# Kernel optimization log

Measured on AMD Instinct MI355X. Metric: run time of the kernel, lower is better.

The kernel has to match this reference:

```python
import jax, jax.numpy as jnp
import numpy as np

B, S, D = 2, 1024, 2048
H, KVH, HD = 16, 4, 128
HID, E, K = 4096, 8, 2
EPS = 1e-5
NEG = -1e9  # finite stand-in for -inf in the causal mask


def setup_inputs() -> dict:
    key = jax.random.key(0)
    ks = jax.random.split(key, 16)
    sc = 0.02
    x = jax.random.normal(ks[0], (B, S, D), jnp.float32)
    # rotary tables (theta = 10000), as cos/sin instead of complex
    inv_freq = 1.0 / (10000.0 ** (jnp.arange(0, HD, 2, dtype=jnp.float32) / HD))
    t = jnp.arange(S, dtype=jnp.float32)
    fr = jnp.outer(t, inv_freq)  # [S, HD/2]
    freqs_cos, freqs_sin = jnp.cos(fr), jnp.sin(fr)
    positions = jnp.arange(S, dtype=jnp.int32)
    mask = jnp.where(jnp.tril(jnp.ones((S, S), bool)), 0.0, NEG).astype(jnp.float32)
    attn_norm_w = jnp.ones((D,), jnp.float32)
    ffn_norm_w = jnp.ones((D,), jnp.float32)
    wq = jax.random.normal(ks[1], (D, H * HD), jnp.float32) * sc
    wk = jax.random.normal(ks[2], (D, KVH * HD), jnp.float32) * sc
    wv = jax.random.normal(ks[3], (D, KVH * HD), jnp.float32) * sc
    wo = jax.random.normal(ks[4], (H * HD, D), jnp.float32) * sc
    gate_w = jax.random.normal(ks[5], (D, E), jnp.float32) * sc
    w1 = jax.random.normal(ks[6], (E, D, HID), jnp.float32) * sc
    w2 = jax.random.normal(ks[7], (E, HID, D), jnp.float32) * sc
    w3 = jax.random.normal(ks[8], (E, D, HID), jnp.float32) * sc
    return dict(x=x, freqs_cos=freqs_cos, freqs_sin=freqs_sin, positions=positions,
                mask=mask, attn_norm_w=attn_norm_w, ffn_norm_w=ffn_norm_w,
                wq=wq, wk=wk, wv=wv, wo=wo, gate_w=gate_w, w1=w1, w2=w2, w3=w3)


def rmsnorm(x, w):
    xf = x.astype(jnp.float32)
    n = xf * jax.lax.rsqrt(jnp.mean(xf * xf, axis=-1, keepdims=True) + EPS)
    return n.astype(x.dtype) * w


def rope(t, cos, sin):
    # t: [B,S,nh,HD]; interleaved (real, imag) pairs like torch.view_as_complex
    tr = t.reshape(*t.shape[:-1], HD // 2, 2)
    xr, xi = tr[..., 0], tr[..., 1]
    c = cos[None, :, None, :]
    s = sin[None, :, None, :]
    out = jnp.stack([xr * c - xi * s, xr * s + xi * c], axis=-1)
    return out.reshape(t.shape)


def block_fwd(x, freqs_cos, freqs_sin, mask, attn_norm_w, ffn_norm_w,
              wq, wk, wv, wo, gate_w, w1, w2, w3):
    # ---- attention ----
    h = rmsnorm(x, attn_norm_w)
    q = (h @ wq).reshape(B, S, H, HD)
    k = (h @ wk).reshape(B, S, KVH, HD)
    v = (h @ wv).reshape(B, S, KVH, HD)
    q = rope(q, freqs_cos, freqs_sin)
    k = rope(k, freqs_cos, freqs_sin)
    rep = H // KVH
    k = jnp.repeat(k, rep, axis=2)  # [B,S,H,HD]
    v = jnp.repeat(v, rep, axis=2)
    scale = HD ** -0.5
    scores = jnp.einsum('bqhd,bkhd->bhqk', q, k) * scale + mask[None, None]
    probs = jax.nn.softmax(scores.astype(jnp.float32), axis=-1).astype(q.dtype)
    attn = jnp.einsum('bhqk,bkhd->bqhd', probs, v).reshape(B, S, H * HD)
    h1 = x + attn @ wo
    # ---- MoE FFN ----
    t = rmsnorm(h1, ffn_norm_w).reshape(-1, D)  # [T,D]
    logits = t @ gate_w  # [T,E]
    topw, sel = jax.lax.top_k(logits, K)
    topw = jax.nn.softmax(topw.astype(jnp.float32), axis=-1).astype(t.dtype)
    out = jnp.zeros_like(t)
    for i in range(E):
        coef = jnp.sum(jnp.where(sel == i, topw, 0.0), axis=-1, keepdims=True)  # [T,1]
        ff = (jax.nn.silu(t @ w1[i]) * (t @ w3[i])) @ w2[i]
        out = out + coef * ff
    return h1 + out.reshape(B, S, D)


def reference(x, freqs_cos, freqs_sin, positions, mask, attn_norm_w, ffn_norm_w,
              wq, wk, wv, wo, gate_w, w1, w2, w3):
    # prefill branch (positions.shape[0] > 1): KV-cache scatter is a write-only
    # side effect in the original and does not affect this output.
    del positions
    return block_fwd(x, freqs_cos, freqs_sin, mask, attn_norm_w, ffn_norm_w,
                     wq, wk, wv, wo, gate_w, w1, w2, w3)
```

## Files before the change

kernel.cpp:

```cpp
#include <hip/hip_runtime.h>

typedef unsigned short u16;
typedef unsigned int u32;
typedef __bf16 bf16x8 __attribute__((ext_vector_type(8)));
typedef _Float16 f16;
typedef f16 f16x8 __attribute__((ext_vector_type(8)));
typedef float f32x4 __attribute__((ext_vector_type(4)));
typedef u32 u32x2 __attribute__((ext_vector_type(2)));

#define DEVFN __device__ __forceinline__

constexpr int kB = 2, kS = 1024, kD = 2048, kH = 16, kKVH = 4, kHD = 128;
constexpr int kHID = 4096, kE = 8;
constexpr int kRows = kB * kS;
constexpr int kQKVN = kH*kHD + 2*kKVH*kHD;
constexpr int kSlotsPad = 5120;
constexpr int kMaxTiles = 40;
constexpr float kEps = 1e-5f;
constexpr float kNeg = -1000000000.0f;
constexpr float kScale = 0.08838834764831845f;

DEVFN u16 f2bf(float f) {
  u32 u = __float_as_uint(f);
  return (u16)((u + 0x7fffu + ((u >> 16) & 1u)) >> 16);
}
DEVFN float bf2f(u16 u) { u32 v = ((u32)u) << 16; return __uint_as_float(v); }

DEVFN void split8v(float4 a, float4 b, f16x8& hi, f16x8& lo) {
  float v[8] = {a.x, a.y, a.z, a.w, b.x, b.y, b.z, b.w};
  #pragma unroll
  for (int e = 0; e < 8; ++e) {
    f16 h = (f16)v[e];
    hi[e] = h;
    lo[e] = (f16)(v[e] - (float)h);
  }
}

DEVFN void gll16(const void* g, void* l) {
  __builtin_amdgcn_global_load_lds(
      (const __attribute__((address_space(1))) void*)g,
      (__attribute__((address_space(3))) void*)l, 16, 0, 0);
}

DEVFN u32x2 pk4bf(float a, float b, float c, float d) {
  union { __bf16 h[4]; u32x2 w; } u;
  u.h[0] = (__bf16)a; u.h[1] = (__bf16)b;
  u.h[2] = (__bf16)c; u.h[3] = (__bf16)d;
  return u.w;
}

__global__ __launch_bounds__(256) void rms_split_kernel(const float* __restrict__ in,
    const float* __restrict__ w, f16* __restrict__ oh, f16* __restrict__ ol) {
  int row = blockIdx.x, tid = threadIdx.x;
  const float* x = in + (size_t)row * kD;
  float4 v0 = *(const float4*)&x[tid*8];
  float4 v1 = *(const float4*)&x[tid*8+4];
  float ss = v0.x*v0.x+v0.y*v0.y+v0.z*v0.z+v0.w*v0.w
           + v1.x*v1.x+v1.y*v1.y+v1.z*v1.z+v1.w*v1.w;
  #pragma unroll
  for (int off = 32; off; off >>= 1) ss += __shfl_xor(ss, off);
  __shared__ float red[4];
  if ((tid & 63) == 0) red[tid >> 6] = ss;
  __syncthreads();
  float tot = red[0] + red[1] + red[2] + red[3];
  float rs = rsqrtf(tot * (1.0f/kD) + kEps);
  float4 w0 = *(const float4*)&w[tid*8];
  float4 w1 = *(const float4*)&w[tid*8+4];
  float4 o0, o1;
  o0.x = v0.x*rs*w0.x; o0.y = v0.y*rs*w0.y; o0.z = v0.z*rs*w0.z; o0.w = v0.w*rs*w0.w;
  o1.x = v1.x*rs*w1.x; o1.y = v1.y*rs*w1.y; o1.z = v1.z*rs*w1.z; o1.w = v1.w*rs*w1.w;
  f16x8 hi, lo;
  split8v(o0, o1, hi, lo);
  *(f16x8*)&oh[(size_t)row*kD + tid*8] = hi;
  *(f16x8*)&ol[(size_t)row*kD + tid*8] = lo;
}

__global__ __launch_bounds__(256) void rms_bf16_kernel(const float* __restrict__ in,
    const float* __restrict__ w, u16* __restrict__ out) {
  int row = blockIdx.x, tid = threadIdx.x;
  const float* x = in + (size_t)row * kD;
  float4 v0 = *(const float4*)&x[tid*8];
  float4 v1 = *(const float4*)&x[tid*8+4];
  float ss = v0.x*v0.x+v0.y*v0.y+v0.z*v0.z+v0.w*v0.w
           + v1.x*v1.x+v1.y*v1.y+v1.z*v1.z+v1.w*v1.w;
  #pragma unroll
  for (int off = 32; off; off >>= 1) ss += __shfl_xor(ss, off);
  __shared__ float red[4];
  if ((tid & 63) == 0) red[tid >> 6] = ss;
  __syncthreads();
  float tot = red[0] + red[1] + red[2] + red[3];
  float rs = rsqrtf(tot * (1.0f/kD) + kEps);
  float4 w0 = *(const float4*)&w[tid*8];
  float4 w1 = *(const float4*)&w[tid*8+4];
  union { int4 i4; u16 u[8]; } pk;
  pk.u[0] = f2bf(v0.x*rs*w0.x); pk.u[1] = f2bf(v0.y*rs*w0.y);
  pk.u[2] = f2bf(v0.z*rs*w0.z); pk.u[3] = f2bf(v0.w*rs*w0.w);
  pk.u[4] = f2bf(v1.x*rs*w1.x); pk.u[5] = f2bf(v1.y*rs*w1.y);
  pk.u[6] = f2bf(v1.z*rs*w1.z); pk.u[7] = f2bf(v1.w*rs*w1.w);
  *(int4*)&out[(size_t)row*kD + tid*8] = pk.i4;
}

__global__ void transpose_split_kernel(const float* __restrict__ in,
    f16* __restrict__ hi, f16* __restrict__ lo, int R, int C, int noff, int ldout) {
  __shared__ float tile[32][33];
  int c0 = blockIdx.x * 32, r0 = blockIdx.y * 32;
  int tx = threadIdx.x, ty = threadIdx.y;
  #pragma unroll
  for (int i = 0; i < 32; i += 8)
    tile[ty + i][tx] = in[(size_t)(r0 + ty + i) * C + c0 + tx];
  __syncthreads();
  #pragma unroll
  for (int i = 0; i < 32; i += 8) {
    float v = tile[tx][ty + i];
    f16 h = (f16)v;
    size_t o = (size_t)(noff + c0 + ty + i) * ldout + r0 + tx;
    hi[o] = h;
    lo[o] = (f16)(v - (float)h);
  }
}

__global__ void vt_split_kernel(const float* __restrict__ qkv,
    f16* __restrict__ vTh, f16* __restrict__ vTl) {
  __shared__ float tile[32][33];
  int s0 = blockIdx.x * 32, c0 = blockIdx.y * 32, b = blockIdx.z;
  int tx = threadIdx.x, ty = threadIdx.y;
  #pragma unroll
  for (int i = 0; i < 32; i += 8)
    tile[ty + i][tx] = qkv[(size_t)(b*kS + s0 + ty + i) * kQKVN + kH*kHD + kKVH*kHD + c0 + tx];
  __syncthreads();
  #pragma unroll
  for (int i = 0; i < 32; i += 8) {
    float v = tile[tx][ty + i];
    f16 h = (f16)v;
    size_t o = (size_t)(b*kKVH*kHD + c0 + ty + i) * kS + s0 + tx;
    vTh[o] = h;
    vTl[o] = (f16)(v - (float)h);
  }
}

template<bool ADDX>
__global__ __launch_bounds__(256) void gemm_sf16_kernel(
    const f16* __restrict__ Ah0, const f16* __restrict__ Al0, int lda,
    const f16* __restrict__ Bh0, const f16* __restrict__ Bl0,
    float* __restrict__ C, int ldc, int coff,
    const float* __restrict__ X, int ldx, int K) {
  __shared__ __align__(16) u16 Ah[128*64], Al[128*64], Bh[128*64], Bl[128*64];
  int tid = threadIdx.x, lane = tid & 63, w = tid >> 6;
  int bm = blockIdx.y * 128, bn = blockIdx.x * 128;
  int wr = w >> 1, wc = w & 1;
  int hg = lane >> 4, lid = lane & 15;
  f32x4 acc[4][4] = {};
  const f16 *aH[4], *aL[4], *bH[4], *bL[4];
  #pragma unroll
  for (int j = 0; j < 4; ++j) {
    int r = w*32 + j*8 + (lane >> 3);
    int colc = ((lane & 7) ^ (r & 7)) * 8;
    aH[j] = Ah0 + (size_t)(bm + r) * lda + colc;
    aL[j] = Al0 + (size_t)(bm + r) * lda + colc;
    bH[j] = Bh0 + (size_t)(bn + r) * K + colc;
    bL[j] = Bl0 + (size_t)(bn + r) * K + colc;
  }
  const char* AhB = (const char*)Ah; const char* AlB = (const char*)Al;
  const char* BhB = (const char*)Bh; const char* BlB = (const char*)Bl;
  for (int kt = 0; kt < K; kt += 64) {
    __syncthreads();
    #pragma unroll
    for (int j = 0; j < 4; ++j) {
      int lb = w*2048 + j*512;
      gll16(aH[j] + kt, &Ah[lb]);
      gll16(aL[j] + kt, &Al[lb]);
      gll16(bH[j] + kt, &Bh[lb]);
      gll16(bL[j] + kt, &Bl[lb]);
    }
    __syncthreads();
    #pragma unroll
    for (int kk = 0; kk < 2; ++kk) {
      f16x8 ah[4], al[4], bh[4], bl[4];
      #pragma unroll
      for (int f = 0; f < 4; ++f) {
        int rA = wr*64 + f*16 + lid;
        int oA = (rA*128 + kk*64 + hg*16) ^ ((rA & 7) << 4);
        ah[f] = *(const f16x8*)(AhB + oA);
        al[f] = *(const f16x8*)(AlB + oA);
        int rB = wc*64 + f*16 + lid;
        int oB = (rB*128 + kk*64 + hg*16) ^ ((rB & 7) << 4);
        bh[f] = *(const f16x8*)(BhB + oB);
        bl[f] = *(const f16x8*)(BlB + oB);
      }
      __builtin_amdgcn_s_setprio(1);
      #pragma unroll
      for (int i = 0; i < 4; ++i)
        #pragma unroll
        for (int j = 0; j < 4; ++j) {
          acc[i][j] = __builtin_amdgcn_mfma_f32_16x16x32_f16(ah[i], bh[j], acc[i][j], 0, 0, 0);
          acc[i][j] = __builtin_amdgcn_mfma_f32_16x16x32_f16(ah[i], bl[j], acc[i][j], 0, 0, 0);
          acc[i][j] = __builtin_amdgcn_mfma_f32_16x16x32_f16(al[i], bh[j], acc[i][j], 0, 0, 0);
        }
      __builtin_amdgcn_s_setprio(0);
    }
  }
  #pragma unroll
  for (int i = 0; i < 4; ++i) {
    #pragma unroll
    for (int rr = 0; rr < 4; ++rr) {
      size_t gr = (size_t)(bm + wr*64 + i*16 + hg*4 + rr);
      #pragma unroll
      for (int j = 0; j < 4; ++j) {
        int gc = bn + wc*64 + j*16 + lid;
        float v = acc[i][j][rr];
        if (ADDX) v += X[gr * ldx + gc];
        C[gr * ldc + coff + gc] = v;
      }
    }
  }
}

__global__ __launch_bounds__(256) void rope_kernel(float* __restrict__ qkv,
    const float* __restrict__ fc, const float* __restrict__ fs,
    f16* __restrict__ Kh, f16* __restrict__ Kl) {
  int idx = blockIdx.x * 256 + threadIdx.x;
  constexpr int NQ = kB*kS*kH*(kHD/2);
  constexpr int NK = kB*kS*kKVH*(kHD/2);
  if (idx < NQ) {
    int i = idx & 63, h = (idx >> 6) & 15, s = (idx >> 10) & 1023, b = idx >> 20;
    size_t base = ((size_t)(b*kS + s))*kQKVN + h*kHD + 2*i;
    float c = fc[s*64 + i], sn = fs[s*64 + i];
    float xr = qkv[base], xi = qkv[base+1];
    qkv[base]   = xr*c - xi*sn;
    qkv[base+1] = xr*sn + xi*c;
  } else {
    int j = idx - NQ; if (j >= NK) return;
    int i = j & 63, h = (j >> 6) & 3, s = (j >> 8) & 1023, b = j >> 18;
    size_t src = ((size_t)(b*kS + s))*kQKVN + kH*kHD + h*kHD + 2*i;
    float c = fc[s*64 + i], sn = fs[s*64 + i];
    float xr = qkv[src], xi = qkv[src+1];
    float o0 = xr*c - xi*sn, o1 = xr*sn + xi*c;
    size_t dst = (((size_t)(b*kKVH + h))*kS + s)*kHD + 2*i;
    f16 h0 = (f16)o0, h1 = (f16)o1;
    Kh[dst]   = h0; Kl[dst]   = (f16)(o0 - (float)h0);
    Kh[dst+1] = h1; Kl[dst+1] = (f16)(o1 - (float)h1);
  }
}

__global__ __launch_bounds__(256) void attn_sf16_kernel(const float* __restrict__ qkv,
    const f16* __restrict__ Ksh, const f16* __restrict__ Ksl,
    const f16* __restrict__ vTh, const f16* __restrict__ vTl,
    f16* __restrict__ outh, f16* __restrict__ outl) {
  int qt = (int)gridDim.x - 1 - blockIdx.x;
  int h = blockIdx.y, b = blockIdx.z;
  int kvh = h >> 2;
  int q0 = qt * 64;
  __shared__ __align__(16) char Kh[64*128*2], Kl[64*128*2];
  __shared__ __align__(16) char Vh[128*64*2], Vl[128*64*2];
  __shared__ __align__(16) char Ph[4][16*64*2], Pl[4][16*64*2];
  int tid = threadIdx.x, lane = tid & 63, w = tid >> 6;
  int hg = lane >> 4, lid = lane & 15;

  f16x8 qh[4], ql[4];
  {
    const float* qrow = qkv + (size_t)(b*kS + q0 + w*16 + lid) * kQKVN + h*kHD;
    #pragma unroll
    for (int ks = 0; ks < 4; ++ks) {
      float4 a = *(const float4*)(qrow + ks*32 + hg*8);
      float4 c = *(const float4*)(qrow + ks*32 + hg*8 + 4);
      split8v(a, c, qh[ks], ql[ks]);
    }
  }
  f32x4 oacc[8] = {};
  float m[4] = {-3.0e38f, -3.0e38f, -3.0e38f, -3.0e38f};
  float lsum[4] = {};
  char* Phw = Ph[w];
  char* Plw = Pl[w];

  for (int kt = 0; kt <= qt; ++kt) {
    __syncthreads();
    {
      int r = tid >> 2, c0 = (tid & 3) * 32;
      const f16* khr = Ksh + ((size_t)(b*kKVH + kvh)*kS + kt*64 + r) * kHD + c0;
      const f16* klr = Ksl + ((size_t)(b*kKVH + kvh)*kS + kt*64 + r) * kHD + c0;
      #pragma unroll
      for (int s8 = 0; s8 < 4; ++s8) {
        int4 hi = *(const int4*)(khr + s8*8);
        int4 lo = *(const int4*)(klr + s8*8);
        int off = (r*256 + c0*2 + s8*16) ^ ((r & 7) << 4);
        *(int4*)(Kh + off) = hi;
        *(int4*)(Kl + off) = lo;
      }
    }
    {
      int r = tid >> 1, c0 = (tid & 1) * 32;
      const f16* vhr = vTh + (size_t)(b*kKVH*kHD + kvh*kHD + r) * kS + kt*64 + c0;
      const f16* vlr = vTl + (size_t)(b*kKVH*kHD + kvh*kHD + r) * kS + kt*64 + c0;
      #pragma unroll
      for (int s8 = 0; s8 < 4; ++s8) {
        int4 hi = *(const int4*)(vhr + s8*8);
        int4 lo = *(const int4*)(vlr + s8*8);
        int off = (r*128 + c0*2 + s8*16) ^ ((r & 7) << 4);
        *(int4*)(Vh + off) = hi;
        *(int4*)(Vl + off) = lo;
      }
    }
    __syncthreads();

    f32x4 sacc[4] = {};
    __builtin_amdgcn_s_setprio(1);
    #pragma unroll
    for (int ks = 0; ks < 4; ++ks) {
      #pragma unroll
      for (int j = 0; j < 4; ++j) {
        int rB = j*16 + lid;
        int off = (rB*256 + ks*64 + hg*16) ^ ((rB & 7) << 4);
        f16x8 kh = *(const f16x8*)(Kh + off);
        f16x8 klo = *(const f16x8*)(Kl + off);
        sacc[j] = __builtin_amdgcn_mfma_f32_16x16x32_f16(qh[ks], kh, sacc[j], 0, 0, 0);
        sacc[j] = __builtin_amdgcn_mfma_f32_16x16x32_f16(qh[ks], klo, sacc[j], 0, 0, 0);
        sacc[j] = __builtin_amdgcn_mfma_f32_16x16x32_f16(ql[ks], kh, sacc[j], 0, 0, 0);
      }
    }
    __builtin_amdgcn_s_setprio(0);
    float s[4][4], ps[4][4];
    bool diag = (kt == qt);
    #pragma unroll
    for (int j = 0; j < 4; ++j)
      #pragma unroll
      for (int r = 0; r < 4; ++r) {
        float v = sacc[j][r] * kScale;
        if (diag) {
          int kvabs = kt*64 + j*16 + lid;
          int qabs = q0 + w*16 + hg*4 + r;
          if (kvabs > qabs) v = kNeg;
        }
        s[j][r] = v;
      }
    float pm[4], cf[4];
    #pragma unroll
    for (int r = 0; r < 4; ++r) {
      pm[r] = fmaxf(fmaxf(s[0][r], s[1][r]), fmaxf(s[2][r], s[3][r]));
      #pragma unroll
      for (int msk = 1; msk < 16; msk <<= 1) pm[r] = fmaxf(pm[r], __shfl_xor(pm[r], msk));
      float mn = fmaxf(m[r], pm[r]);
      cf[r] = __expf(m[r] - mn);
      m[r] = mn;
    }
    #pragma unroll
    for (int j2 = 0; j2 < 8; ++j2)
      #pragma unroll
      for (int r = 0; r < 4; ++r) oacc[j2][r] *= cf[r];
    float rs[4] = {};
    #pragma unroll
    for (int j = 0; j < 4; ++j)
      #pragma unroll
      for (int r = 0; r < 4; ++r) {
        float p = __expf(s[j][r] - m[r]);
        ps[j][r] = p;
        rs[r] += p;
      }
    #pragma unroll
    for (int r = 0; r < 4; ++r) lsum[r] = lsum[r]*cf[r] + rs[r];
    #pragma unroll
    for (int j = 0; j < 4; ++j)
      #pragma unroll
      for (int r = 0; r < 4; ++r) {
        int q = hg*4 + r;
        int off = (q*128 + (j*16 + lid)*2) ^ ((q & 7) << 4);
        f16 ph = (f16)ps[j][r];
        *(f16*)(Phw + off) = ph;
        *(f16*)(Plw + off) = (f16)(ps[j][r] - (float)ph);
      }
    #pragma unroll
    for (int kk2 = 0; kk2 < 2; ++kk2) {
      int oP = (lid*128 + kk2*64 + hg*16) ^ ((lid & 7) << 4);
      f16x8 pa_h = *(const f16x8*)(Phw + oP);
      f16x8 pa_l = *(const f16x8*)(Plw + oP);
      __builtin_amdgcn_s_setprio(1);
      #pragma unroll
      for (int j2 = 0; j2 < 8; ++j2) {
        int rV = j2*16 + lid;
        int off = (rV*128 + kk2*64 + hg*16) ^ ((rV & 7) << 4);
        f16x8 vh = *(const f16x8*)(Vh + off);
        f16x8 vl = *(const f16x8*)(Vl + off);
        oacc[j2] = __builtin_amdgcn_mfma_f32_16x16x32_f16(pa_h, vh, oacc[j2], 0, 0, 0);
        oacc[j2] = __builtin_amdgcn_mfma_f32_16x16x32_f16(pa_h, vl, oacc[j2], 0, 0, 0);
        oacc[j2] = __builtin_amdgcn_mfma_f32_16x16x32_f16(pa_l, vh, oacc[j2], 0, 0, 0);
      }
      __builtin_amdgcn_s_setprio(0);
    }
  }
  #pragma unroll
  for (int r = 0; r < 4; ++r) {
    #pragma unroll
    for (int msk = 1; msk < 16; msk <<= 1) lsum[r] += __shfl_xor(lsum[r], msk);
    lsum[r] = 1.f / lsum[r];
  }
  #pragma unroll
  for (int j2 = 0; j2 < 8; ++j2)
    #pragma unroll
    for (int r = 0; r < 4; ++r) {
      size_t o = (size_t)(b*kS + q0 + w*16 + hg*4 + r) * kD + h*kHD + j2*16 + lid;
      float v = oacc[j2][r] * lsum[r];
      f16 hh = (f16)v;
      outh[o] = hh;
      outl[o] = (f16)(v - (float)hh);
    }
}

__global__ void zero_counts_kernel(int* counts) {
  if (threadIdx.x < kE) counts[threadIdx.x] = 0;
}

__global__ __launch_bounds__(64) void gate_kernel(const float* __restrict__ h1,
    const float* __restrict__ wn, const float* __restrict__ gw,
    int* __restrict__ packA, int* __restrict__ packB,
    float* __restrict__ cA, float* __restrict__ cB,
    int* __restrict__ lists, int* __restrict__ counts) {
  int row = blockIdx.x, lane = threadIdx.x;
  const float* x = h1 + (size_t)row * kD;
  float ss = 0.f;
  for (int d = lane; d < kD; d += 64) { float v = x[d]; ss = fmaf(v, v, ss); }
  #pragma unroll
  for (int off = 32; off; off >>= 1) ss += __shfl_xor(ss, off);
  float rs = rsqrtf(ss * (1.0f/kD) + kEps);
  float acc[kE] = {};
  for (int d = lane; d < kD; d += 64) {
    float g = x[d] * rs * wn[d];
    const float* gr = gw + (size_t)d * kE;
    #pragma unroll
    for (int e = 0; e < kE; ++e) acc[e] = fmaf(g, gr[e], acc[e]);
  }
  #pragma unroll
  for (int e = 0; e < kE; ++e)
    #pragma unroll
    for (int off = 32; off; off >>= 1) acc[e] += __shfl_xor(acc[e], off);
  if (lane == 0) {
    int i1 = 0; float l1 = acc[0];
    #pragma unroll
    for (int e = 1; e < kE; ++e) if (acc[e] > l1) { l1 = acc[e]; i1 = e; }
    int i2 = -1; float l2 = -3.4e38f;
    #pragma unroll
    for (int e = 0; e < kE; ++e) if (e != i1 && acc[e] > l2) { l2 = acc[e]; i2 = e; }
    float e2 = __expf(l2 - l1);
    float inv = 1.f / (1.f + e2);
    int p1 = atomicAdd(&counts[i1], 1); lists[i1*kRows + p1] = row;
    int p2 = atomicAdd(&counts[i2], 1); lists[i2*kRows + p2] = row;
    packA[row] = i1*2048 + p1; cA[row] = inv;
    packB[row] = i2*2048 + p2; cB[row] = e2 * inv;
  }
}

__global__ void prefix_kernel(const int* __restrict__ counts,
    int* __restrict__ padbase, int* __restrict__ tileTab) {
  if (threadIdx.x == 0) {
    int base = 0, idx = 0;
    for (int e = 0; e < kE; ++e) {
      padbase[e] = base;
      int nt = (counts[e] + 127) >> 7;
      for (int t = 0; t < nt; ++t) tileTab[idx++] = (e << 8) | t;
      base += nt << 7;
    }
    for (; idx < kMaxTiles; ++idx) tileTab[idx] = -1;
  }
}

__global__ __launch_bounds__(256) void gemm_up_kernel(
    const u16* __restrict__ A, const float* __restrict__ W1, const float* __restrict__ W3,
    u16* __restrict__ hid, const int* __restrict__ lists,
    const int* __restrict__ counts, const int* __restrict__ padbase,
    const int* __restrict__ tileTab) {
  int tab = tileTab[blockIdx.y];
  if (tab < 0) return;
  int e = tab >> 8, mb = tab & 255;
  int cnt = counts[e];
  int bm = mb * 128;
  int slot0 = padbase[e] + bm;
  const int* ids = lists + e * kRows;
  int g = blockIdx.x;
  __shared__ __align__(16) char SM[65536];
  u16* As[2]   = { (u16*)SM, (u16*)(SM + 16384) };
  char* B1s[2] = { SM + 32768, SM + 40960 };
  char* B3s[2] = { SM + 49152, SM + 57344 };
  int tid = threadIdx.x, lane = tid & 63, w = tid >> 6;
  int wr = w >> 1, wc = w & 1;
  int hg = lane >> 4, lid = lane & 15;
  f32x4 acc[4][4] = {};

  const u16* aP[4];
  #pragma unroll
  for (int j = 0; j < 4; ++j) {
    int r = w*32 + j*8 + (lane >> 3);
    int colc = ((lane & 7) ^ (r & 7)) * 8;
    int rr = bm + r; if (rr >= cnt) rr = cnt - 1;
    aP[j] = A + (size_t)ids[rr] * kD + colc;
  }
  const float* b1e = W1 + (size_t)e*kD*kHID + (size_t)g*64 + lane;
  const float* b3e = W3 + (size_t)e*kD*kHID + (size_t)g*64 + lane;
  int wOff[4];
  #pragma unroll
  for (int s = 0; s < 4; ++s)
    wOff[s] = (lane*128 + s*32 + w*8) ^ ((lane & 7) << 4);

  auto stageA = [&](int buf, int t) {
    int kt = t * 64;
    #pragma unroll
    for (int j = 0; j < 4; ++j) gll16(aP[j] + kt, &As[buf][w*2048 + j*512]);
  };
  float r1v[4][4], r3v[4][4];
  auto loadB = [&](int t) {
    int kt = t * 64;
    #pragma unroll
    for (int s = 0; s < 4; ++s)
      #pragma unroll
      for (int j = 0; j < 4; ++j) {
        size_t ko = (size_t)(kt + s*16 + w*4 + j) * kHID;
        r1v[s][j] = b1e[ko];
        r3v[s][j] = b3e[ko];
      }
  };
  auto writeB = [&](int buf) {
    #pragma unroll
    for (int s = 0; s < 4; ++s) {
      *(u32x2*)(B1s[buf] + wOff[s]) = pk4bf(r1v[s][0], r1v[s][1], r1v[s][2], r1v[s][3]);
      *(u32x2*)(B3s[buf] + wOff[s]) = pk4bf(r3v[s][0], r3v[s][1], r3v[s][2], r3v[s][3]);
    }
  };
  auto compute = [&](int buf) {
    const char* AsB = (const char*)As[buf];
    const char* Bb = wc ? B3s[buf] : B1s[buf];
    #pragma unroll
    for (int kk = 0; kk < 2; ++kk) {
      bf16x8 af[4], bfv[4];
      #pragma unroll
      for (int f = 0; f < 4; ++f) {
        int rA = wr*64 + f*16 + lid;
        af[f] = *(const bf16x8*)(AsB + ((rA*128 + kk*64 + hg*16) ^ ((rA & 7) << 4)));
        int rB = f*16 + lid;
        bfv[f] = *(const bf16x8*)(Bb + ((rB*128 + kk*64 + hg*16) ^ ((rB & 7) << 4)));
      }
      __builtin_amdgcn_s_setprio(1);
      #pragma unroll
      for (int i = 0; i < 4; ++i)
        #pragma unroll
        for (int j = 0; j < 4; ++j)
          acc[i][j] = __builtin_amdgcn_mfma_f32_16x16x32_bf16(af[i], bfv[j], acc[i][j], 0, 0, 0);
      __builtin_amdgcn_s_setprio(0);
    }
  };

  constexpr int NT = kD / 64;
  stageA(0, 0);
  loadB(0);
  writeB(0);
  __syncthreads();
  for (int t = 0; t < NT; t += 2) {
    stageA(1, t+1); loadB(t+1);
    compute(0);
    writeB(1);
    __syncthreads();
    if (t+2 < NT) { stageA(0, t+2); loadB(t+2); }
    compute(1);
    if (t+2 < NT) writeB(0);
    __syncthreads();
  }

  float* Xch = (float*)SM;
  if (wc == 0) {
    #pragma unroll
    for (int i = 0; i < 4; ++i)
      #pragma unroll
      for (int rr = 0; rr < 4; ++rr) {
        int row = wr*64 + i*16 + hg*4 + rr;
        #pragma unroll
        for (int j = 0; j < 4; ++j)
          Xch[row*64 + j*16 + lid] = acc[i][j][rr];
      }
  }
  __syncthreads();
  if (wc == 1) {
    #pragma unroll
    for (int i = 0; i < 4; ++i)
      #pragma unroll
      for (int rr = 0; rr < 4; ++rr) {
        int row = wr*64 + i*16 + hg*4 + rr;
        int gr = bm + row;
        if (gr >= cnt) continue;
        u16* orow = hid + (size_t)(slot0 + row) * kHID + g*64;
        #pragma unroll
        for (int j = 0; j < 4; ++j) {
          int col = j*16 + lid;
          float g1 = Xch[row*64 + col];
          float g3 = acc[i][j][rr];
          orow[col] = f2bf(g1 / (1.f + __expf(-g1)) * g3);
        }
      }
  }
}

__global__ __launch_bounds__(256) void gemm_down_kernel(
    const u16* __restrict__ hid, const float* __restrict__ W2,
    u16* __restrict__ ff, const int* __restrict__ padbase,
    const int* __restrict__ tileTab) {
  int tab = tileTab[blockIdx.y];
  if (tab < 0) return;
  int e = tab >> 8, mb = tab & 255;
  int slot0 = padbase[e] + mb * 128;
  int bn = blockIdx.x * 128;
  __shared__ __align__(16) char SM[65536];
  u16* As[2] = { (u16*)SM, (u16*)(SM + 16384) };
  char* Bs[2] = { SM + 32768, SM + 49152 };
  int tid = threadIdx.x, lane = tid & 63, w = tid >> 6;
  int wr = w >> 1, wc = w & 1;
  int hg = lane >> 4, lid = lane & 15;
  f32x4 acc[4][4] = {};

  const u16* aP[4];
  #pragma unroll
  for (int j = 0; j < 4; ++j) {
    int r = w*32 + j*8 + (lane >> 3);
    int colc = ((lane & 7) ^ (r & 7)) * 8;
    aP[j] = hid + (size_t)(slot0 + r) * kHID + colc;
  }
  int nrow = (w & 1)*64 + lane;
  int kq = w >> 1;
  const float* b2e = W2 + (size_t)e*kHID*kD + (size_t)bn + nrow;
  int wOff[8];
  #pragma unroll
  for (int s = 0; s < 8; ++s)
    wOff[s] = (nrow*128 + s*16 + kq*8) ^ ((nrow & 7) << 4);

  auto stageA = [&](int buf, int t) {
    int kt = t * 64;
    #pragma unroll
    for (int j = 0; j < 4; ++j) gll16(aP[j] + kt, &As[buf][w*2048 + j*512]);
  };
  float rbv[8][4];
  auto loadB = [&](int t) {
    int kt = t * 64;
    #pragma unroll
    for (int s = 0; s < 8; ++s)
      #pragma unroll
      for (int j = 0; j < 4; ++j)
        rbv[s][j] = b2e[(size_t)(kt + s*8 + kq*4 + j) * kD];
  };
  auto writeB = [&](int buf) {
    #pragma unroll
    for (int s = 0; s < 8; ++s)
      *(u32x2*)(Bs[buf] + wOff[s]) = pk4bf(rbv[s][0], rbv[s][1], rbv[s][2], rbv[s][3]);
  };
  auto compute = [&](int buf) {
    const char* AsB = (const char*)As[buf];
    const char* Bb = Bs[buf];
    #pragma unroll
    for (int kk = 0; kk < 2; ++kk) {
      bf16x8 af[4], bfv[4];
      #pragma unroll
      for (int f = 0; f < 4; ++f) {
        int rA = wr*64 + f*16 + lid;
        af[f] = *(const bf16x8*)(AsB + ((rA*128 + kk*64 + hg*16) ^ ((rA & 7) << 4)));
        int rB = wc*64 + f*16 + lid;
        bfv[f] = *(const bf16x8*)(Bb + ((rB*128 + kk*64 + hg*16) ^ ((rB & 7) << 4)));
      }
      __builtin_amdgcn_s_setprio(1);
      #pragma unroll
      for (int i = 0; i < 4; ++i)
        #pragma unroll
        for (int j = 0; j < 4; ++j)
          acc[i][j] = __builtin_amdgcn_mfma_f32_16x16x32_bf16(af[i], bfv[j], acc[i][j], 0, 0, 0);
      __builtin_amdgcn_s_setprio(0);
    }
  };

  constexpr int NT = kHID / 64;
  stageA(0, 0);
  loadB(0);
  writeB(0);
  __syncthreads();
  for (int t = 0; t < NT; t += 2) {
    stageA(1, t+1); loadB(t+1);
    compute(0);
    writeB(1);
    __syncthreads();
    if (t+2 < NT) { stageA(0, t+2); loadB(t+2); }
    compute(1);
    if (t+2 < NT) writeB(0);
    __syncthreads();
  }

  #pragma unroll
  for (int i = 0; i < 4; ++i)
    #pragma unroll
    for (int rr = 0; rr < 4; ++rr) {
      int row = wr*64 + i*16 + hg*4 + rr;
      u16* orow = ff + (size_t)(slot0 + row) * kD + bn;
      #pragma unroll
      for (int j = 0; j < 4; ++j)
        orow[wc*64 + j*16 + lid] = f2bf(acc[i][j][rr]);
    }
}

__global__ __launch_bounds__(256) void moe_combine_kernel(
    const u16* __restrict__ ff, const int* __restrict__ padbase,
    const int* __restrict__ packA, const int* __restrict__ packB,
    const float* __restrict__ cA, const float* __restrict__ cB,
    float* __restrict__ outp) {
  int row = blockIdx.x, tid = threadIdx.x;
  int pa = packA[row], pb = packB[row];
  int sa = padbase[pa >> 11] + (pa & 2047);
  int sb = padbase[pb >> 11] + (pb & 2047);
  float ca = cA[row], cb = cB[row];
  union { int4 i4; u16 u[8]; } va, vb;
  va.i4 = *(const int4*)(ff + (size_t)sa * kD + tid*8);
  vb.i4 = *(const int4*)(ff + (size_t)sb * kD + tid*8);
  float* o = outp + (size_t)row * kD + tid*8;
  float4 o0 = *(const float4*)o;
  float4 o1 = *(const float4*)(o + 4);
  o0.x += ca*bf2f(va.u[0]) + cb*bf2f(vb.u[0]);
  o0.y += ca*bf2f(va.u[1]) + cb*bf2f(vb.u[1]);
  o0.z += ca*bf2f(va.u[2]) + cb*bf2f(vb.u[2]);
  o0.w += ca*bf2f(va.u[3]) + cb*bf2f(vb.u[3]);
  o1.x += ca*bf2f(va.u[4]) + cb*bf2f(vb.u[4]);
  o1.y += ca*bf2f(va.u[5]) + cb*bf2f(vb.u[5]);
  o1.z += ca*bf2f(va.u[6]) + cb*bf2f(vb.u[6]);
  o1.w += ca*bf2f(va.u[7]) + cb*bf2f(vb.u[7]);
  *(float4*)o = o0;
  *(float4*)(o + 4) = o1;
}

extern "C" void kernel_launch(void* const* d_in, const int* in_sizes, int n_in,
                              void* d_out, int out_size, void* d_ws, size_t ws_size,
                              hipStream_t stream) {
  const float* x    = (const float*)d_in[0];
  const float* fcos = (const float*)d_in[1];
  const float* fsin = (const float*)d_in[2];
  const float* anw  = (const float*)d_in[5];
  const float* fnw  = (const float*)d_in[6];
  const float* wq   = (const float*)d_in[7];
  const float* wk   = (const float*)d_in[8];
  const float* wv   = (const float*)d_in[9];
  const float* wo   = (const float*)d_in[10];
  const float* gw   = (const float*)d_in[11];
  const float* w1   = (const float*)d_in[12];
  const float* w2   = (const float*)d_in[13];
  const float* w3   = (const float*)d_in[14];
  float* outp = (float*)d_out;

  char* ws = (char*)d_ws;
  size_t off = 0;
  auto alloc = [&](size_t bytes) -> void* {
    void* p = ws + off; off += (bytes + 255) & ~(size_t)255; return p;
  };
  f16* h16h   = (f16*)alloc((size_t)kRows*kD*2);
  f16* h16l   = (f16*)alloc((size_t)kRows*kD*2);
  float* qkv  = (float*)alloc((size_t)kRows*kQKVN*4);
  f16* Ksh    = (f16*)alloc((size_t)kB*kKVH*kS*kHD*2);
  f16* Ksl    = (f16*)alloc((size_t)kB*kKVH*kS*kHD*2);
  f16* vTh    = (f16*)alloc((size_t)kB*kKVH*kHD*kS*2);
  f16* vTl    = (f16*)alloc((size_t)kB*kKVH*kHD*kS*2);
  f16* a16h   = (f16*)alloc((size_t)kRows*kD*2);
  f16* a16l   = (f16*)alloc((size_t)kRows*kD*2);
  u16* tbf    = (u16*)alloc((size_t)kRows*kD*2);
  int* packA  = (int*)alloc(kRows*4);
  int* packB  = (int*)alloc(kRows*4);
  float* cAv  = (float*)alloc(kRows*4);
  float* cBv  = (float*)alloc(kRows*4);
  int* counts = (int*)alloc(kE*4);
  int* padbase= (int*)alloc(kE*4);
  int* tileTab= (int*)alloc(kMaxTiles*4);
  int* lists  = (int*)alloc((size_t)kE*kRows*4);
  f16* Bqh    = (f16*)alloc((size_t)kQKVN*kD*2);
  f16* Bql    = (f16*)alloc((size_t)kQKVN*kD*2);
  f16* Bwh    = (f16*)alloc((size_t)kD*kD*2);
  f16* Bwl    = (f16*)alloc((size_t)kD*kD*2);
  u16* hid    = (u16*)alloc((size_t)kSlotsPad*kHID*2);
  u16* ffb    = (u16*)alloc((size_t)kSlotsPad*kD*2);

  transpose_split_kernel<<<dim3(kD/32, kD/32), dim3(32,8), 0, stream>>>(wq, Bqh, Bql, kD, 2048, 0, kD);
  transpose_split_kernel<<<dim3(512/32, kD/32), dim3(32,8), 0, stream>>>(wk, Bqh, Bql, kD, 512, 2048, kD);
  transpose_split_kernel<<<dim3(512/32, kD/32), dim3(32,8), 0, stream>>>(wv, Bqh, Bql, kD, 512, 2560, kD);
  transpose_split_kernel<<<dim3(kD/32, kD/32), dim3(32,8), 0, stream>>>(wo, Bwh, Bwl, kD, kD, 0, kD);

  rms_split_kernel<<<kRows, 256, 0, stream>>>(x, anw, h16h, h16l);
  gemm_sf16_kernel<false><<<dim3(kQKVN/128, kRows/128), 256, 0, stream>>>(
      h16h, h16l, kD, Bqh, Bql, qkv, kQKVN, 0, nullptr, 0, kD);
  rope_kernel<<<(kB*kS*(kH+kKVH)*(kHD/2))/256, 256, 0, stream>>>(qkv, fcos, fsin, Ksh, Ksl);
  vt_split_kernel<<<dim3(kS/32, (kKVH*kHD)/32, kB), dim3(32,8), 0, stream>>>(qkv, vTh, vTl);
  attn_sf16_kernel<<<dim3(kS/64, kH, kB), 256, 0, stream>>>(qkv, Ksh, Ksl, vTh, vTl, a16h, a16l);
  gemm_sf16_kernel<true><<<dim3(kD/128, kRows/128), 256, 0, stream>>>(
      a16h, a16l, kD, Bwh, Bwl, outp, kD, 0, x, kD, kD);

  zero_counts_kernel<<<1, 64, 0, stream>>>(counts);
  gate_kernel<<<kRows, 64, 0, stream>>>(outp, fnw, gw, packA, packB, cAv, cBv, lists, counts);
  prefix_kernel<<<1, 64, 0, stream>>>(counts, padbase, tileTab);
  rms_bf16_kernel<<<kRows, 256, 0, stream>>>(outp, fnw, tbf);

  gemm_up_kernel<<<dim3(kHID/64, kMaxTiles), 256, 0, stream>>>(
      tbf, w1, w3, hid, lists, counts, padbase, tileTab);
  gemm_down_kernel<<<dim3(kD/128, kMaxTiles), 256, 0, stream>>>(
      hid, w2, ffb, padbase, tileTab);
  moe_combine_kernel<<<kRows, 256, 0, stream>>>(
      ffb, padbase, packA, packB, cAv, cBv, outp);
}
```

Measured before the change: 866.6 us.

## Deepen MoE GEMM weight prefetch with float2 loads and explicit waitcnt barriers

In both MoE expert GEMM kernels, the fp32 weight loads now fetch two adjacent columns per thread as float2, which halves the number of global load instructions. The weights for the next tile are held in two register sets (even and odd), so they are loaded one full tile ahead. The loop uses hand-placed s_barrier calls with explicit vmcnt and lgkmcnt waits and sched_barrier fences, so outstanding global loads can overlap compute instead of draining at every __syncthreads. In exchange this needs more registers, and correctness now depends on the hard-coded vmcnt(20) count matching the real number of loads in flight.

New measurement: 1.134 ms. 30.9% more time.

```diff
diff --git a/kernel.cpp b/kernel.cpp
--- a/kernel.cpp
+++ b/kernel.cpp
@@ -48,6 +48,22 @@
   u.h[2] = (__bf16)c; u.h[3] = (__bf16)d;
   return u.w;
 }
+
+DEVFN void baronly() { __builtin_amdgcn_sched_barrier(0);
+  __builtin_amdgcn_s_barrier();
+  __builtin_amdgcn_sched_barrier(0); }
+DEVFN void barlgkm() { __builtin_amdgcn_sched_barrier(0);
+  asm volatile("s_waitcnt lgkmcnt(0)" ::: "memory");
+  __builtin_amdgcn_s_barrier();
+  __builtin_amdgcn_sched_barrier(0); }
+DEVFN void barvm20() { __builtin_amdgcn_sched_barrier(0);
+  asm volatile("s_waitcnt vmcnt(20) lgkmcnt(0)" ::: "memory");
+  __builtin_amdgcn_s_barrier();
+  __builtin_amdgcn_sched_barrier(0); }
+DEVFN void barvm0() { __builtin_amdgcn_sched_barrier(0);
+  asm volatile("s_waitcnt vmcnt(0) lgkmcnt(0)" ::: "memory");
+  __builtin_amdgcn_s_barrier();
+  __builtin_amdgcn_sched_barrier(0); }
 
 __global__ __launch_bounds__(256) void rms_split_kernel(const float* __restrict__ in,
     const float* __restrict__ w, f16* __restrict__ oh, f16* __restrict__ ol) {
@@ -491,35 +507,39 @@
     int rr = bm + r; if (rr >= cnt) rr = cnt - 1;
     aP[j] = A + (size_t)ids[rr] * kD + colc;
   }
-  const float* b1e = W1 + (size_t)e*kD*kHID + (size_t)g*64 + lane;
-  const float* b3e = W3 + (size_t)e*kD*kHID + (size_t)g*64 + lane;
-  int wOff[4];
-  #pragma unroll
-  for (int s = 0; s < 4; ++s)
-    wOff[s] = (lane*128 + s*32 + w*8) ^ ((lane & 7) << 4);
+  int c0 = (tid & 31) * 2, hk = tid >> 5;
+  const float* b1e = W1 + (size_t)e*kD*kHID + (size_t)g*64 + c0;
+  const float* b3e = W3 + (size_t)e*kD*kHID + (size_t)g*64 + c0;
+  int wOffX[2], wOffY[2];
+  #pragma unroll
+  for (int q = 0; q < 2; ++q) {
+    int k0b = (hk*8 + q*4) * 2;
+    wOffX[q] = (c0*128 + k0b) ^ ((c0 & 7) << 4);
+    wOffY[q] = ((c0+1)*128 + k0b) ^ (((c0+1) & 7) << 4);
+  }
+  float2 r1E[8], r3E[8], r1O[8], r3O[8];
 
   auto stageA = [&](int buf, int t) {
     int kt = t * 64;
     #pragma unroll
     for (int j = 0; j < 4; ++j) gll16(aP[j] + kt, &As[buf][w*2048 + j*512]);
   };
-  float r1v[4][4], r3v[4][4];
-  auto loadB = [&](int t) {
+  auto loadB = [&](float2* r1, float2* r3, int t) {
     int kt = t * 64;
     #pragma unroll
-    for (int s = 0; s < 4; ++s)
-      #pragma unroll
-      for (int j = 0; j < 4; ++j) {
-        size_t ko = (size_t)(kt + s*16 + w*4 + j) * kHID;
-        r1v[s][j] = b1e[ko];
-        r3v[s][j] = b3e[ko];
-      }
+    for (int j = 0; j < 8; ++j) {
+      size_t ko = (size_t)(kt + hk*8 + j) * kHID;
+      r1[j] = *(const float2*)(b1e + ko);
+      r3[j] = *(const float2*)(b3e + ko);
+    }
   };
-  auto writeB = [&](int buf) {
-    #pragma unroll
-    for (int s = 0; s < 4; ++s) {
-      *(u32x2*)(B1s[buf] + wOff[s]) = pk4bf(r1v[s][0], r1v[s][1], r1v[s][2], r1v[s][3]);
-      *(u32x2*)(B3s[buf] + wOff[s]) = pk4bf(r3v[s][0], r3v[s][1], r3v[s][2], r3v[s][3]);
+  auto writeB = [&](int buf, float2* r1, float2* r3) {
+    #pragma unroll
+    for (int q = 0; q < 2; ++q) {
+      *(u32x2*)(B1s[buf] + wOffX[q]) = pk4bf(r1[q*4].x, r1[q*4+1].x, r1[q*4+2].x, r1[q*4+3].x);
+      *(u32x2*)(B1s[buf] + wOffY[q]) = pk4bf(r1[q*4].y, r1[q*4+1].y, r1[q*4+2].y, r1[q*4+3].y);
+      *(u32x2*)(B3s[buf] + wOffX[q]) = pk4bf(r3[q*4].x, r3[q*4+1].x, r3[q*4+2].x, r3[q*4+3].x);
+      *(u32x2*)(B3s[buf] + wOffY[q]) = pk4bf(r3[q*4].y, r3[q*4+1].y, r3[q*4+2].y, r3[q*4+3].y);
     }
   };
   auto compute = [&](int buf) {
@@ -546,20 +566,31 @@
   };
 
   constexpr int NT = kD / 64;
-  stageA(0, 0);
-  loadB(0);
-  writeB(0);
+  stageA(0, 0); stageA(1, 1);
+  loadB(r1E, r3E, 0);
+  loadB(r1O, r3O, 1);
+  writeB(0, r1E, r3E);
+  barlgkm();
+  for (int t = 0; t + 2 < NT; t += 2) {
+    loadB(r1E, r3E, t+2);
+    compute(0);
+    baronly();
+    stageA(0, t+2);
+    writeB(1, r1O, r3O);
+    barvm20();
+    loadB(r1O, r3O, t+3);
+    compute(1);
+    baronly();
+    stageA(1, t+3);
+    writeB(0, r1E, r3E);
+    barvm20();
+  }
+  compute(0);
+  baronly();
+  writeB(1, r1O, r3O);
+  barvm0();
+  compute(1);
   __syncthreads();
-  for (int t = 0; t < NT; t += 2) {
-    stageA(1, t+1); loadB(t+1);
-    compute(0);
-    writeB(1);
-    __syncthreads();
-    if (t+2 < NT) { stageA(0, t+2); loadB(t+2); }
-    compute(1);
-    if (t+2 < NT) writeB(0);
-    __syncthreads();
-  }
 
   float* Xch = (float*)SM;
   if (wc == 0) {
@@ -618,32 +649,34 @@
     int colc = ((lane & 7) ^ (r & 7)) * 8;
     aP[j] = hid + (size_t)(slot0 + r) * kHID + colc;
   }
-  int nrow = (w & 1)*64 + lane;
-  int kq = w >> 1;
-  const float* b2e = W2 + (size_t)e*kHID*kD + (size_t)bn + nrow;
-  int wOff[8];
-  #pragma unroll
-  for (int s = 0; s < 8; ++s)
-    wOff[s] = (nrow*128 + s*16 + kq*8) ^ ((nrow & 7) << 4);
+  int c0 = (tid & 63) * 2, kgrp = tid >> 6;
+  const float* b2e = W2 + (size_t)e*kHID*kD + (size_t)bn + c0;
+  int wOffX[4], wOffY[4];
+  #pragma unroll
+  for (int q = 0; q < 4; ++q) {
+    int k0b = (kgrp*16 + q*4) * 2;
+    wOffX[q] = (c0*128 + k0b) ^ ((c0 & 7) << 4);
+    wOffY[q] = ((c0+1)*128 + k0b) ^ (((c0+1) & 7) << 4);
+  }
+  float2 rE[16], rO[16];
 
   auto stageA = [&](int buf, int t) {
     int kt = t * 64;
     #pragma unroll
     for (int j = 0; j < 4; ++j) gll16(aP[j] + kt, &As[buf][w*2048 + j*512]);
   };
-  float rbv[8][4];
-  auto loadB = [&](int t) {
+  auto loadB = [&](float2* r, int t) {
     int kt = t * 64;
     #pragma unroll
-    for (int s = 0; s < 8; ++s)
-      #pragma unroll
-      for (int j = 0; j < 4; ++j)
-        rbv[s][j] = b2e[(size_t)(kt + s*8 + kq*4 + j) * kD];
+    for (int j = 0; j < 16; ++j)
+      r[j] = *(const float2*)(b2e + (size_t)(kt + kgrp*16 + j) * kD);
   };
-  auto writeB = [&](int buf) {
-    #pragma unroll
-    for (int s = 0; s < 8; ++s)
-      *(u32x2*)(Bs[buf] + wOff[s]) = pk4bf(rbv[s][0], rbv[s][1], rbv[s][2], rbv[s][3]);
+  auto writeB = [&](int buf, float2* r) {
+    #pragma unroll
+    for (int q = 0; q < 4; ++q) {
+      *(u32x2*)(Bs[buf] + wOffX[q]) = pk4bf(r[q*4].x, r[q*4+1].x, r[q*4+2].x, r[q*4+3].x);
+      *(u32x2*)(Bs[buf] + wOffY[q]) = pk4bf(r[q*4].y, r[q*4+1].y, r[q*4+2].y, r[q*4+3].y);
+    }
   };
   auto compute = [&](int buf) {
     const char* AsB = (const char*)As[buf];
@@ -669,20 +702,31 @@
   };
 
   constexpr int NT = kHID / 64;
-  stageA(0, 0);
-  loadB(0);
-  writeB(0);
+  stageA(0, 0); stageA(1, 1);
+  loadB(rE, 0);
+  loadB(rO, 1);
+  writeB(0, rE);
+  barlgkm();
+  for (int t = 0; t + 2 < NT; t += 2) {
+    loadB(rE, t+2);
+    compute(0);
+    baronly();
+    stageA(0, t+2);
+    writeB(1, rO);
+    barvm20();
+    loadB(rO, t+3);
+    compute(1);
+    baronly();
+    stageA(1, t+3);
+    writeB(0, rE);
+    barvm20();
+  }
+  compute(0);
+  baronly();
+  writeB(1, rO);
+  barvm0();
+  compute(1);
   __syncthreads();
-  for (int t = 0; t < NT; t += 2) {
-    stageA(1, t+1); loadB(t+1);
-    compute(0);
-    writeB(1);
-    __syncthreads();
-    if (t+2 < NT) { stageA(0, t+2); loadB(t+2); }
-    compute(1);
-    if (t+2 < NT) writeB(0);
-    __syncthreads();
-  }
 
   #pragma unroll
   for (int i = 0; i < 4; ++i)
```

## Use 8 waves per block in MoE up/down GEMMs with smaller per-wave tiles

Applied to the files above, without the earlier changes.

Doubles the threads per block in the expert up- and down-projection GEMMs from 256 to 512 and re-splits the 128-wide tile so each wave computes a 64x32 sub-tile instead of 64x64. The A-staging and fp32-to-bf16 weight loads are divided over twice as many threads. The aim is more waves in flight to hide the global-load latency of the fp32 weights and fewer registers per thread. In exchange, each wave does less MFMA work per LDS fragment load, and the launch bound of 4 blocks per CU with 64KB of LDS per block may not be reachable.

After: 864.0 us (median of 2 runs). About the same (-0.3%).

```diff
diff --git a/kernel.cpp b/kernel.cpp
--- a/kernel.cpp
+++ b/kernel.cpp
@@ -461,7 +461,7 @@
   }
 }
 
-__global__ __launch_bounds__(256) void gemm_up_kernel(
+__global__ __launch_bounds__(512, 4) void gemm_up_kernel(
     const u16* __restrict__ A, const float* __restrict__ W1, const float* __restrict__ W3,
     u16* __restrict__ hid, const int* __restrict__ lists,
     const int* __restrict__ counts, const int* __restrict__ padbase,
@@ -479,67 +479,70 @@
   char* B1s[2] = { SM + 32768, SM + 40960 };
   char* B3s[2] = { SM + 49152, SM + 57344 };
   int tid = threadIdx.x, lane = tid & 63, w = tid >> 6;
-  int wr = w >> 1, wc = w & 1;
+  int wr = w >> 2, wcc = w & 3;
   int hg = lane >> 4, lid = lane & 15;
-  f32x4 acc[4][4] = {};
-
-  const u16* aP[4];
-  #pragma unroll
-  for (int j = 0; j < 4; ++j) {
-    int r = w*32 + j*8 + (lane >> 3);
+  f32x4 acc[4][2] = {};
+
+  const u16* aP[2];
+  #pragma unroll
+  for (int j = 0; j < 2; ++j) {
+    int r = w*16 + j*8 + (lane >> 3);
     int colc = ((lane & 7) ^ (r & 7)) * 8;
     int rr = bm + r; if (rr >= cnt) rr = cnt - 1;
     aP[j] = A + (size_t)ids[rr] * kD + colc;
   }
   const float* b1e = W1 + (size_t)e*kD*kHID + (size_t)g*64 + lane;
   const float* b3e = W3 + (size_t)e*kD*kHID + (size_t)g*64 + lane;
-  int wOff[4];
-  #pragma unroll
-  for (int s = 0; s < 4; ++s)
-    wOff[s] = (lane*128 + s*32 + w*8) ^ ((lane & 7) << 4);
+  int wOff[2];
+  #pragma unroll
+  for (int s = 0; s < 2; ++s)
+    wOff[s] = (lane*128 + w*16 + s*8) ^ ((lane & 7) << 4);
 
   auto stageA = [&](int buf, int t) {
     int kt = t * 64;
     #pragma unroll
-    for (int j = 0; j < 4; ++j) gll16(aP[j] + kt, &As[buf][w*2048 + j*512]);
+    for (int j = 0; j < 2; ++j) gll16(aP[j] + kt, &As[buf][w*1024 + j*512]);
   };
-  float r1v[4][4], r3v[4][4];
+  float r1v[2][4], r3v[2][4];
   auto loadB = [&](int t) {
     int kt = t * 64;
     #pragma unroll
-    for (int s = 0; s < 4; ++s)
+    for (int s = 0; s < 2; ++s)
       #pragma unroll
       for (int j = 0; j < 4; ++j) {
-        size_t ko = (size_t)(kt + s*16 + w*4 + j) * kHID;
+        size_t ko = (size_t)(kt + w*8 + s*4 + j) * kHID;
         r1v[s][j] = b1e[ko];
         r3v[s][j] = b3e[ko];
       }
   };
   auto writeB = [&](int buf) {
     #pragma unroll
-    for (int s = 0; s < 4; ++s) {
+    for (int s = 0; s < 2; ++s) {
       *(u32x2*)(B1s[buf] + wOff[s]) = pk4bf(r1v[s][0], r1v[s][1], r1v[s][2], r1v[s][3]);
       *(u32x2*)(B3s[buf] + wOff[s]) = pk4bf(r3v[s][0], r3v[s][1], r3v[s][2], r3v[s][3]);
     }
   };
   auto compute = [&](int buf) {
     const char* AsB = (const char*)As[buf];
-    const char* Bb = wc ? B3s[buf] : B1s[buf];
+    const char* Bb = (wcc >= 2) ? B3s[buf] : B1s[buf];
     #pragma unroll
     for (int kk = 0; kk < 2; ++kk) {
-      bf16x8 af[4], bfv[4];
+      bf16x8 af[4], bfv[2];
       #pragma unroll
       for (int f = 0; f < 4; ++f) {
         int rA = wr*64 + f*16 + lid;
         af[f] = *(const bf16x8*)(AsB + ((rA*128 + kk*64 + hg*16) ^ ((rA & 7) << 4)));
-        int rB = f*16 + lid;
+      }
+      #pragma unroll
+      for (int f = 0; f < 2; ++f) {
+        int rB = (wcc & 1)*32 + f*16 + lid;
         bfv[f] = *(const bf16x8*)(Bb + ((rB*128 + kk*64 + hg*16) ^ ((rB & 7) << 4)));
       }
       __builtin_amdgcn_s_setprio(1);
       #pragma unroll
       for (int i = 0; i < 4; ++i)
         #pragma unroll
-        for (int j = 0; j < 4; ++j)
+        for (int j = 0; j < 2; ++j)
           acc[i][j] = __builtin_amdgcn_mfma_f32_16x16x32_bf16(af[i], bfv[j], acc[i][j], 0, 0, 0);
       __builtin_amdgcn_s_setprio(0);
     }
@@ -562,19 +565,19 @@
   }
 
   float* Xch = (float*)SM;
-  if (wc == 0) {
+  if (wcc < 2) {
     #pragma unroll
     for (int i = 0; i < 4; ++i)
       #pragma unroll
       for (int rr = 0; rr < 4; ++rr) {
         int row = wr*64 + i*16 + hg*4 + rr;
         #pragma unroll
-        for (int j = 0; j < 4; ++j)
-          Xch[row*64 + j*16 + lid] = acc[i][j][rr];
+        for (int j = 0; j < 2; ++j)
+          Xch[row*64 + (wcc & 1)*32 + j*16 + lid] = acc[i][j][rr];
       }
   }
   __syncthreads();
-  if (wc == 1) {
+  if (wcc >= 2) {
     #pragma unroll
     for (int i = 0; i < 4; ++i)
       #pragma unroll
@@ -582,11 +585,11 @@
         int row = wr*64 + i*16 + hg*4 + rr;
         int gr = bm + row;
         if (gr >= cnt) continue;
-        u16* orow = hid + (size_t)(slot0 + row) * kHID + g*64;
+        u16* orow = hid + (size_t)(slot0 + row) * kHID + g*64 + (wcc & 1)*32;
         #pragma unroll
-        for (int j = 0; j < 4; ++j) {
+        for (int j = 0; j < 2; ++j) {
           int col = j*16 + lid;
-          float g1 = Xch[row*64 + col];
+          float g1 = Xch[row*64 + (wcc & 1)*32 + col];
           float g3 = acc[i][j][rr];
           orow[col] = f2bf(g1 / (1.f + __expf(-g1)) * g3);
         }
@@ -594,7 +597,7 @@
   }
 }
 
-__global__ __launch_bounds__(256) void gemm_down_kernel(
+__global__ __launch_bounds__(512, 4) void gemm_down_kernel(
     const u16* __restrict__ hid, const float* __restrict__ W2,
     u16* __restrict__ ff, const int* __restrict__ padbase,
     const int* __restrict__ tileTab) {
@@ -607,42 +610,42 @@
   u16* As[2] = { (u16*)SM, (u16*)(SM + 16384) };
   char* Bs[2] = { SM + 32768, SM + 49152 };
   int tid = threadIdx.x, lane = tid & 63, w = tid >> 6;
-  int wr = w >> 1, wc = w & 1;
+  int wr = w >> 2, wc = w & 3;
   int hg = lane >> 4, lid = lane & 15;
-  f32x4 acc[4][4] = {};
-
-  const u16* aP[4];
-  #pragma unroll
-  for (int j = 0; j < 4; ++j) {
-    int r = w*32 + j*8 + (lane >> 3);
+  f32x4 acc[4][2] = {};
+
+  const u16* aP[2];
+  #pragma unroll
+  for (int j = 0; j < 2; ++j) {
+    int r = w*16 + j*8 + (lane >> 3);
     int colc = ((lane & 7) ^ (r & 7)) * 8;
     aP[j] = hid + (size_t)(slot0 + r) * kHID + colc;
   }
-  int nrow = (w & 1)*64 + lane;
-  int kq = w >> 1;
+  int nrow = tid & 127;
+  int kq = tid >> 7;
   const float* b2e = W2 + (size_t)e*kHID*kD + (size_t)bn + nrow;
-  int wOff[8];
-  #pragma unroll
-  for (int s = 0; s < 8; ++s)
-    wOff[s] = (nrow*128 + s*16 + kq*8) ^ ((nrow & 7) << 4);
+  int wOff[4];
+  #pragma unroll
+  for (int s = 0; s < 4; ++s)
+    wOff[s] = (nrow*128 + kq*32 + s*8) ^ ((nrow & 7) << 4);
 
   auto stageA = [&](int buf, int t) {
     int kt = t * 64;
     #pragma unroll
-    for (int j = 0; j < 4; ++j) gll16(aP[j] + kt, &As[buf][w*2048 + j*512]);
+    for (int j = 0; j < 2; ++j) gll16(aP[j] + kt, &As[buf][w*1024 + j*512]);
   };
-  float rbv[8][4];
+  float rbv[4][4];
   auto loadB = [&](int t) {
     int kt = t * 64;
     #pragma unroll
-    for (int s = 0; s < 8; ++s)
+    for (int s = 0; s < 4; ++s)
       #pragma unroll
       for (int j = 0; j < 4; ++j)
-        rbv[s][j] = b2e[(size_t)(kt + s*8 + kq*4 + j) * kD];
+        rbv[s][j] = b2e[(size_t)(kt + kq*16 + s*4 + j) * kD];
   };
   auto writeB = [&](int buf) {
     #pragma unroll
-    for (int s = 0; s < 8; ++s)
+    for (int s = 0; s < 4; ++s)
       *(u32x2*)(Bs[buf] + wOff[s]) = pk4bf(rbv[s][0], rbv[s][1], rbv[s][2], rbv[s][3]);
   };
   auto compute = [&](int buf) {
@@ -650,19 +653,22 @@
     const char* Bb = Bs[buf];
     #pragma unroll
     for (int kk = 0; kk < 2; ++kk) {
-      bf16x8 af[4], bfv[4];
+      bf16x8 af[4], bfv[2];
       #pragma unroll
       for (int f = 0; f < 4; ++f) {
         int rA = wr*64 + f*16 + lid;
         af[f] = *(const bf16x8*)(AsB + ((rA*128 + kk*64 + hg*16) ^ ((rA & 7) << 4)));
-        int rB = wc*64 + f*16 + lid;
+      }
+      #pragma unroll
+      for (int f = 0; f < 2; ++f) {
+        int rB = wc*32 + f*16 + lid;
         bfv[f] = *(const bf16x8*)(Bb + ((rB*128 + kk*64 + hg*16) ^ ((rB & 7) << 4)));
       }
       __builtin_amdgcn_s_setprio(1);
       #pragma unroll
       for (int i = 0; i < 4; ++i)
         #pragma unroll
-        for (int j = 0; j < 4; ++j)
+        for (int j = 0; j < 2; ++j)
           acc[i][j] = __builtin_amdgcn_mfma_f32_16x16x32_bf16(af[i], bfv[j], acc[i][j], 0, 0, 0);
       __builtin_amdgcn_s_setprio(0);
     }
@@ -691,8 +697,8 @@
       int row = wr*64 + i*16 + hg*4 + rr;
       u16* orow = ff + (size_t)(slot0 + row) * kD + bn;
       #pragma unroll
-      for (int j = 0; j < 4; ++j)
-        orow[wc*64 + j*16 + lid] = f2bf(acc[i][j][rr]);
+      for (int j = 0; j < 2; ++j)
+        orow[wc*32 + j*16 + lid] = f2bf(acc[i][j][rr]);
     }
 }
 
@@ -791,9 +797,9 @@
   prefix_kernel<<<1, 64, 0, stream>>>(counts, padbase, tileTab);
   rms_bf16_kernel<<<kRows, 256, 0, stream>>>(outp, fnw, tbf);
 
-  gemm_up_kernel<<<dim3(kHID/64, kMaxTiles), 256, 0, stream>>>(
+  gemm_up_kernel<<<dim3(kHID/64, kMaxTiles), 512, 0, stream>>>(
       tbf, w1, w3, hid, lists, counts, padbase, tileTab);
-  gemm_down_kernel<<<dim3(kD/128, kMaxTiles), 256, 0, stream>>>(
+  gemm_down_kernel<<<dim3(kD/128, kMaxTiles), 512, 0, stream>>>(
       hid, w2, ffb, padbase, tileTab);
   moe_combine_kernel<<<kRows, 256, 0, stream>>>(
       ffb, padbase, packA, packB, cAv, cBv, outp);
```
